# Kernel tuning notes

Hardware: AMD Instinct MI355X
Metric: run time of the kernel (lower is better)

The kernel has to match this reference:

```python
import jax, jax.numpy as jnp
import numpy as np

VOCAB, D_IN, D_H, D_OUT = 32000, 512, 1024, 32000
B, S = 64, 512

def setup_inputs() -> dict:
    key = jax.random.key(0)
    ks = jax.random.split(key, 6)
    xav = lambda k, shp: jax.random.uniform(k, shp, jnp.float32, -1.0, 1.0) * np.sqrt(6.0 / (shp[0] + shp[1]))
    return {
        "tokens": jax.random.randint(ks[0], (B, S), 0, VOCAB),
        "h0": jnp.zeros((B, D_H), jnp.float32),
        "embed_table": jax.random.normal(ks[1], (VOCAB, D_IN), jnp.float32),
        "W_ih": xav(ks[2], (D_IN, D_H)),
        "W_hh": xav(ks[3], (D_H, D_H)),
        "bias_hh": jnp.zeros((D_H,), jnp.float32),
        "W_out": xav(ks[4], (D_H, D_OUT)),
        "b_out": jnp.zeros((D_OUT,), jnp.float32),
    }

def reference(tokens, h0, embed_table, W_ih, W_hh, bias_hh, W_out, b_out):
    # embed: [B,S,D_in] -> seq-first [S,B,D_in]
    x = embed_table[tokens].transpose(1, 0, 2)
    # precompute input projection for all timesteps (one big GEMM)
    xw = jnp.einsum("sbi,ih->sbh", x, W_ih) + bias_hh

    def step(h, xw_t):
        h_new = jnp.tanh(xw_t + h @ W_hh)
        return h_new, None

    h_last, _ = jax.lax.scan(step, h0, xw)
    y_pred = h_last @ W_out + b_out  # [B, D_OUT]
    return y_pred
```

## Files before the change

kernel.cpp:

```cpp
#include <hip/hip_runtime.h>

#define D_IN 512
#define D_H 1024
#define D_OUT 32000
#define NB 64
#define NS 512

typedef __attribute__((ext_vector_type(8))) short short8;
typedef __attribute__((ext_vector_type(8))) __bf16 bf16x8;
typedef __attribute__((ext_vector_type(4))) float f32x4;

__device__ __forceinline__ unsigned short f2bf(float f) {
  unsigned int u = __float_as_uint(f);
  u += 0x7fffu + ((u >> 16) & 1u);
  return (unsigned short)(u >> 16);
}
__device__ __forceinline__ float bf2f(unsigned short s) {
  return __uint_as_float(((unsigned int)s) << 16);
}

__device__ __forceinline__ f32x4 mfma_bf16(short8 a, short8 b, f32x4 c) {
  return __builtin_amdgcn_mfma_f32_16x16x32_bf16(
      __builtin_bit_cast(bf16x8, a), __builtin_bit_cast(bf16x8, b), c, 0, 0, 0);
}

union HQ { unsigned long long q[2]; short8 s; };

__global__ __launch_bounds__(256) void rnn_init(const float* __restrict__ h0,
                                                unsigned short* __restrict__ hex,
                                                unsigned int* __restrict__ flags) {
  int idx = blockIdx.x * 256 + threadIdx.x;
  int bg = idx >> 10;
  int k = idx & 1023;
  int g = bg >> 4, bl = bg & 15;
  float v = h0[idx];
  unsigned short hh = f2bf(v);
  unsigned short hl = f2bf(v - bf2f(hh));
  size_t base = ((size_t)(g * 2 + 0) * 2) * 16384 + (size_t)bl * 1024 + k;
  hex[base] = hh;
  hex[base + 16384] = hl;
  if (blockIdx.x == 0) flags[threadIdx.x] = 0u;
}

__global__ __launch_bounds__(256) void rnn_pack_wih(const float* __restrict__ W_ih,
                                                    unsigned short* __restrict__ bhi,
                                                    unsigned short* __restrict__ blo) {
  int idx = blockIdx.x * 256 + threadIdx.x;
  int j = idx & 7;
  int l = (idx >> 3) & 63;
  int kc = (idx >> 9) & 15;
  int nc = idx >> 13;
  int k = kc * 32 + ((l >> 4) << 3) + j;
  int n = nc * 16 + (l & 15);
  float v = W_ih[(size_t)k * D_H + n];
  unsigned short h = f2bf(v);
  bhi[idx] = h;
  blo[idx] = f2bf(v - bf2f(h));
}

__global__ __launch_bounds__(256) void rnn_stage1(const int* __restrict__ tokens,
                                                  const float* __restrict__ embed,
                                                  const unsigned short* __restrict__ bhi,
                                                  const unsigned short* __restrict__ blo,
                                                  const float* __restrict__ bias,
                                                  float* __restrict__ xw) {
  int bx = blockIdx.x;
  int mt = bx >> 4, nt = bx & 15;
  int tid = threadIdx.x;
  int w = tid >> 6, l = tid & 63;
  int q = l >> 4;

  int m = mt * 64 + w * 16 + (l & 15);
  int b = m & 63, t = m >> 6;
  int tok = tokens[b * NS + t];
  const float* arow = embed + (size_t)tok * D_IN;

  f32x4 acc[4];
#pragma unroll
  for (int i = 0; i < 4; ++i) acc[i] = (f32x4){0.f, 0.f, 0.f, 0.f};

  for (int c = 0; c < 16; ++c) {
    const float* ap = arow + c * 32 + q * 8;
    float4 f0 = *(const float4*)ap;
    float4 f1 = *(const float4*)(ap + 4);
    float fa[8] = {f0.x, f0.y, f0.z, f0.w, f1.x, f1.y, f1.z, f1.w};
    short8 ahi, alo;
#pragma unroll
    for (int j = 0; j < 8; ++j) {
      unsigned short hh = f2bf(fa[j]);
      ahi[j] = (short)hh;
      alo[j] = (short)f2bf(fa[j] - bf2f(hh));
    }
#pragma unroll
    for (int ni = 0; ni < 4; ++ni) {
      int ncg = nt * 4 + ni;
      size_t boff = ((size_t)(ncg * 16 + c) * 64 + l) * 8;
      short8 bh = *(const short8*)(bhi + boff);
      short8 bl_ = *(const short8*)(blo + boff);
      acc[ni] = mfma_bf16(ahi, bh, acc[ni]);
      acc[ni] = mfma_bf16(alo, bh, acc[ni]);
      acc[ni] = mfma_bf16(ahi, bl_, acc[ni]);
    }
  }

#pragma unroll
  for (int ni = 0; ni < 4; ++ni) {
    int col = nt * 64 + ni * 16 + (l & 15);
    float bv = bias[col];
#pragma unroll
    for (int r = 0; r < 4; ++r) {
      int row = mt * 64 + w * 16 + q * 4 + r;
      xw[(size_t)row * D_H + col] = acc[ni][r] + bv;
    }
  }
}

__global__ __launch_bounds__(256, 1) void rnn_recur(const float* __restrict__ xw,
                                                    const float* __restrict__ W_hh,
                                                    unsigned short* __restrict__ hex,
                                                    unsigned int* __restrict__ flags,
                                                    float* __restrict__ h_last) {
  __shared__ short Whi[32768];
  __shared__ short Wlo[32768];
  __shared__ float red[4][16][33];

  const int tid = threadIdx.x;
  const int bx = blockIdx.x;
  const int g = bx >> 5;
  const int jt = bx & 31;
  const int jcol0 = jt * 32;
  const int w = tid >> 6;
  const int l = tid & 63;
  const int q = l >> 4;
  const int b_lane = l & 15;

  for (int v = tid; v < 32768; v += 256) {
    int j = v & 7;
    int ll = (v >> 3) & 63;
    int c = (v >> 9) & 31;
    int s = v >> 14;
    int k = c * 32 + ((ll >> 4) << 3) + j;
    int n = s * 16 + (ll & 15);
    float wv = W_hh[(size_t)k * D_H + jcol0 + n];
    unsigned short hh = f2bf(wv);
    Whi[v] = (short)hh;
    Wlo[v] = (short)f2bf(wv - bf2f(hh));
  }
  __syncthreads();

  unsigned int* flg = flags + g * 32;

  const int be = tid >> 4;
  const int je2 = (tid & 15) * 2;
  const int brow = g * 16 + be;

  for (int t = 1; t <= NS; ++t) {
    const float* xwp = xw + ((size_t)(t - 1) * 64 + brow) * D_H + jcol0 + je2;
    float xv0 = xwp[0];
    float xv1 = xwp[1];

    if (tid < 64) {
      unsigned int target = (unsigned int)(t - 1);
      while (1) {
        unsigned int v = __hip_atomic_load(&flg[l & 31], __ATOMIC_RELAXED,
                                           __HIP_MEMORY_SCOPE_AGENT);
        if (__all((int)(v >= target))) break;
      }
    }
    __syncthreads();

    int rbuf = (t - 1) & 1;
    const unsigned long long* hhi =
        (const unsigned long long*)(hex + ((size_t)(g * 2 + rbuf) * 2 + 0) * 16384);
    const unsigned long long* hlo =
        (const unsigned long long*)(hex + ((size_t)(g * 2 + rbuf) * 2 + 1) * 16384);

    HQ ha[8], hl_[8];
#pragma unroll
    for (int i = 0; i < 8; ++i) {
      int c = w * 8 + i;
      int k = c * 32 + q * 8;
      size_t qi = ((size_t)b_lane * 1024 + k) >> 2;
      ha[i].q[0] = __hip_atomic_load(hhi + qi, __ATOMIC_RELAXED, __HIP_MEMORY_SCOPE_AGENT);
      ha[i].q[1] = __hip_atomic_load(hhi + qi + 1, __ATOMIC_RELAXED, __HIP_MEMORY_SCOPE_AGENT);
      hl_[i].q[0] = __hip_atomic_load(hlo + qi, __ATOMIC_RELAXED, __HIP_MEMORY_SCOPE_AGENT);
      hl_[i].q[1] = __hip_atomic_load(hlo + qi + 1, __ATOMIC_RELAXED, __HIP_MEMORY_SCOPE_AGENT);
    }

    f32x4 a00 = {0.f, 0.f, 0.f, 0.f}, a01 = a00, a02 = a00;
    f32x4 a10 = a00, a11 = a00, a12 = a00;
#pragma unroll
    for (int i = 0; i < 8; ++i) {
      int c = w * 8 + i;
      short8 bh0 = *(const short8*)(Whi + c * 512 + l * 8);
      short8 bl0 = *(const short8*)(Wlo + c * 512 + l * 8);
      short8 bh1 = *(const short8*)(Whi + 16384 + c * 512 + l * 8);
      short8 bl1 = *(const short8*)(Wlo + 16384 + c * 512 + l * 8);
      a00 = mfma_bf16(ha[i].s, bh0, a00);
      a01 = mfma_bf16(hl_[i].s, bh0, a01);
      a02 = mfma_bf16(ha[i].s, bl0, a02);
      a10 = mfma_bf16(ha[i].s, bh1, a10);
      a11 = mfma_bf16(hl_[i].s, bh1, a11);
      a12 = mfma_bf16(ha[i].s, bl1, a12);
    }
    f32x4 s0 = a00 + a01 + a02;
    f32x4 s1 = a10 + a11 + a12;
#pragma unroll
    for (int r = 0; r < 4; ++r) {
      red[w][q * 4 + r][b_lane] = s0[r];
      red[w][q * 4 + r][16 + b_lane] = s1[r];
    }
    __syncthreads();

    float z0 = red[0][be][je2] + red[1][be][je2] + red[2][be][je2] +
               red[3][be][je2] + xv0;
    float z1 = red[0][be][je2 + 1] + red[1][be][je2 + 1] + red[2][be][je2 + 1] +
               red[3][be][je2 + 1] + xv1;
    float hv0 = tanhf(z0);
    float hv1 = tanhf(z1);
    unsigned short h0h = f2bf(hv0), h1h = f2bf(hv1);
    unsigned short h0l = f2bf(hv0 - bf2f(h0h)), h1l = f2bf(hv1 - bf2f(h1h));
    int wbuf = t & 1;
    size_t obase = (size_t)be * 1024 + jcol0 + je2;
    unsigned int* dhi =
        (unsigned int*)(hex + ((size_t)(g * 2 + wbuf) * 2 + 0) * 16384 + obase);
    unsigned int* dlo =
        (unsigned int*)(hex + ((size_t)(g * 2 + wbuf) * 2 + 1) * 16384 + obase);
    unsigned int phi = (unsigned int)h0h | ((unsigned int)h1h << 16);
    unsigned int plo = (unsigned int)h0l | ((unsigned int)h1l << 16);
    __hip_atomic_store(dhi, phi, __ATOMIC_RELAXED, __HIP_MEMORY_SCOPE_AGENT);
    __hip_atomic_store(dlo, plo, __ATOMIC_RELAXED, __HIP_MEMORY_SCOPE_AGENT);
    if (t == NS) {
      h_last[(size_t)brow * 1024 + jcol0 + je2] = hv0;
      h_last[(size_t)brow * 1024 + jcol0 + je2 + 1] = hv1;
    }

    asm volatile("s_waitcnt vmcnt(0)" ::: "memory");
    __syncthreads();
    if (tid == 0)
      __hip_atomic_store(&flg[jt], (unsigned int)t, __ATOMIC_RELAXED,
                         __HIP_MEMORY_SCOPE_AGENT);
  }
}

__global__ __launch_bounds__(256, 2) void rnn_out(const float* __restrict__ h_last,
                                                  const float* __restrict__ W_out,
                                                  const float* __restrict__ b_out,
                                                  float* __restrict__ out) {
  __shared__ float smem[16384];
  int tid = threadIdx.x;
  int jl = tid & 127;
  int kh = tid >> 7;
  int j = blockIdx.x * 128 + jl;

  float acc[64];
#pragma unroll
  for (int b = 0; b < 64; ++b) acc[b] = 0.f;

  for (int kc = 0; kc < 4; ++kc) {
    __syncthreads();
    for (int v = tid; v < 16384; v += 256) {
      int kh2 = v >> 13;
      int b = (v >> 7) & 63;
      int kk = v & 127;
      smem[v] = h_last[(size_t)b * 1024 + kh2 * 512 + kc * 128 + kk];
    }
    __syncthreads();
    int kbase = kh * 512 + kc * 128;
    for (int kkc = 0; kkc < 16; ++kkc) {
      float wreg[8];
#pragma unroll
      for (int i = 0; i < 8; ++i)
        wreg[i] = W_out[(size_t)(kbase + kkc * 8 + i) * D_OUT + j];
#pragma unroll
      for (int b = 0; b < 64; ++b) {
        const float* hp = &smem[kh * 8192 + b * 128 + kkc * 8];
#pragma unroll
        for (int i = 0; i < 8; ++i) acc[b] += hp[i] * wreg[i];
      }
    }
  }
  __syncthreads();
  if (kh == 1) {
#pragma unroll
    for (int b = 0; b < 64; ++b) smem[jl * 65 + b] = acc[b];
  }
  __syncthreads();
  if (kh == 0) {
    float bo = b_out[j];
#pragma unroll
    for (int b = 0; b < 64; ++b)
      out[(size_t)b * D_OUT + j] = acc[b] + smem[jl * 65 + b] + bo;
  }
}

extern "C" void kernel_launch(void* const* d_in, const int* in_sizes, int n_in,
                              void* d_out, int out_size, void* d_ws, size_t ws_size,
                              hipStream_t stream) {
  const int* tokens = (const int*)d_in[0];
  const float* h0 = (const float*)d_in[1];
  const float* embed = (const float*)d_in[2];
  const float* W_ih = (const float*)d_in[3];
  const float* W_hh = (const float*)d_in[4];
  const float* bias_hh = (const float*)d_in[5];
  const float* W_out = (const float*)d_in[6];
  const float* b_out = (const float*)d_in[7];
  float* out = (float*)d_out;

  char* ws = (char*)d_ws;
  float* xw = (float*)(ws);
  unsigned short* wih_hi = (unsigned short*)(ws + 134217728);
  unsigned short* wih_lo = (unsigned short*)(ws + 135266304);
  unsigned short* hex = (unsigned short*)(ws + 136314880);
  unsigned int* flags = (unsigned int*)(ws + 136839168);
  float* h_last = (float*)(ws + 136840192);

  rnn_init<<<256, 256, 0, stream>>>(h0, hex, flags);
  rnn_pack_wih<<<2048, 256, 0, stream>>>(W_ih, wih_hi, wih_lo);
  rnn_stage1<<<8192, 256, 0, stream>>>(tokens, embed, wih_hi, wih_lo, bias_hh, xw);
  rnn_recur<<<128, 256, 0, stream>>>(xw, W_hh, hex, flags, h_last);
  rnn_out<<<250, 256, 0, stream>>>(h_last, W_out, b_out, out);
}
```

Measured before the change: 3.592 ms.

## Consume hidden-state chunks as producer flags arrive instead of waiting for all

Each wave now polls only the eight producer flags for the K-chunks it consumes. It loads and runs MFMAs on whichever chunks are ready, rather than the whole block spinning until all 32 producers finish and then syncing. The hidden-state exchange buffer is re-laid out so that each producer's 32-column slice, with its hi and lo parts, is contiguous at 2 KB per chunk. The xw load for the next step is prefetched during the previous step. This overlaps computation with the remaining synchronisation wait, but adds a dynamic, masked loop that may raise register pressure and branching.

```diff
diff --git a/kernel.cpp b/kernel.cpp
--- a/kernel.cpp
+++ b/kernel.cpp
@@ -33,12 +33,13 @@
   int bg = idx >> 10;
   int k = idx & 1023;
   int g = bg >> 4, bl = bg & 15;
+  int c = k >> 5, kk = k & 31;
   float v = h0[idx];
   unsigned short hh = f2bf(v);
   unsigned short hl = f2bf(v - bf2f(hh));
-  size_t base = ((size_t)(g * 2 + 0) * 2) * 16384 + (size_t)bl * 1024 + k;
+  size_t base = (size_t)(g * 2) * 32768 + (size_t)c * 1024 + bl * 32 + kk;
   hex[base] = hh;
-  hex[base + 16384] = hl;
+  hex[base + 512] = hl;
   if (blockIdx.x == 0) flags[threadIdx.x] = 0u;
 }
 
@@ -149,60 +150,71 @@
   __syncthreads();
 
   unsigned int* flg = flags + g * 32;
+  const int fidx = w * 8 + (l & 7);
+  const unsigned own = ((jt >> 3) == w) ? (1u << (jt & 7)) : 0u;
+  const int loff = b_lane * 64 + q * 16;
 
   const int be = tid >> 4;
   const int je2 = (tid & 15) * 2;
   const int brow = g * 16 + be;
 
+  char* hexb = (char*)hex;
+
+  float xv0, xv1;
+  {
+    const float* xwp = xw + ((size_t)0 * 64 + brow) * D_H + jcol0 + je2;
+    xv0 = xwp[0];
+    xv1 = xwp[1];
+  }
+
   for (int t = 1; t <= NS; ++t) {
-    const float* xwp = xw + ((size_t)(t - 1) * 64 + brow) * D_H + jcol0 + je2;
-    float xv0 = xwp[0];
-    float xv1 = xwp[1];
-
-    if (tid < 64) {
-      unsigned int target = (unsigned int)(t - 1);
-      while (1) {
-        unsigned int v = __hip_atomic_load(&flg[l & 31], __ATOMIC_RELAXED,
-                                           __HIP_MEMORY_SCOPE_AGENT);
-        if (__all((int)(v >= target))) break;
-      }
-    }
-    __syncthreads();
-
-    int rbuf = (t - 1) & 1;
-    const unsigned long long* hhi =
-        (const unsigned long long*)(hex + ((size_t)(g * 2 + rbuf) * 2 + 0) * 16384);
-    const unsigned long long* hlo =
-        (const unsigned long long*)(hex + ((size_t)(g * 2 + rbuf) * 2 + 1) * 16384);
-
-    HQ ha[8], hl_[8];
-#pragma unroll
-    for (int i = 0; i < 8; ++i) {
-      int c = w * 8 + i;
-      int k = c * 32 + q * 8;
-      size_t qi = ((size_t)b_lane * 1024 + k) >> 2;
-      ha[i].q[0] = __hip_atomic_load(hhi + qi, __ATOMIC_RELAXED, __HIP_MEMORY_SCOPE_AGENT);
-      ha[i].q[1] = __hip_atomic_load(hhi + qi + 1, __ATOMIC_RELAXED, __HIP_MEMORY_SCOPE_AGENT);
-      hl_[i].q[0] = __hip_atomic_load(hlo + qi, __ATOMIC_RELAXED, __HIP_MEMORY_SCOPE_AGENT);
-      hl_[i].q[1] = __hip_atomic_load(hlo + qi + 1, __ATOMIC_RELAXED, __HIP_MEMORY_SCOPE_AGENT);
-    }
+    const unsigned target = (unsigned)(t - 1);
+    const char* hb = hexb + (size_t)(g * 2 + ((t - 1) & 1)) * 65536;
 
     f32x4 a00 = {0.f, 0.f, 0.f, 0.f}, a01 = a00, a02 = a00;
     f32x4 a10 = a00, a11 = a00, a12 = a00;
-#pragma unroll
-    for (int i = 0; i < 8; ++i) {
-      int c = w * 8 + i;
-      short8 bh0 = *(const short8*)(Whi + c * 512 + l * 8);
-      short8 bl0 = *(const short8*)(Wlo + c * 512 + l * 8);
-      short8 bh1 = *(const short8*)(Whi + 16384 + c * 512 + l * 8);
-      short8 bl1 = *(const short8*)(Wlo + 16384 + c * 512 + l * 8);
-      a00 = mfma_bf16(ha[i].s, bh0, a00);
-      a01 = mfma_bf16(hl_[i].s, bh0, a01);
-      a02 = mfma_bf16(ha[i].s, bl0, a02);
-      a10 = mfma_bf16(ha[i].s, bh1, a10);
-      a11 = mfma_bf16(hl_[i].s, bh1, a11);
-      a12 = mfma_bf16(ha[i].s, bl1, a12);
-    }
+
+    unsigned done = 0u;
+    while (done != 255u) {
+      unsigned int fv = __hip_atomic_load(&flg[fidx], __ATOMIC_RELAXED,
+                                          __HIP_MEMORY_SCOPE_AGENT);
+      unsigned rdy = (((unsigned)__ballot((int)(fv >= target))) & 255u) | own;
+      unsigned avail = rdy & ~done;
+      if (avail == 0u) continue;
+      done |= avail;
+
+      HQ ha_[8], hl_[8];
+#pragma unroll
+      for (int i = 0; i < 8; ++i) {
+        if (avail & (1u << i)) {
+          const char* cb = hb + (size_t)(w * 8 + i) * 2048;
+          const unsigned long long* ph = (const unsigned long long*)(cb + loff);
+          const unsigned long long* pl = (const unsigned long long*)(cb + 1024 + loff);
+          ha_[i].q[0] = __hip_atomic_load(ph, __ATOMIC_RELAXED, __HIP_MEMORY_SCOPE_AGENT);
+          ha_[i].q[1] = __hip_atomic_load(ph + 1, __ATOMIC_RELAXED, __HIP_MEMORY_SCOPE_AGENT);
+          hl_[i].q[0] = __hip_atomic_load(pl, __ATOMIC_RELAXED, __HIP_MEMORY_SCOPE_AGENT);
+          hl_[i].q[1] = __hip_atomic_load(pl + 1, __ATOMIC_RELAXED, __HIP_MEMORY_SCOPE_AGENT);
+        }
+      }
+      __builtin_amdgcn_sched_barrier(0);
+#pragma unroll
+      for (int i = 0; i < 8; ++i) {
+        if (avail & (1u << i)) {
+          int c = w * 8 + i;
+          short8 bh0 = *(const short8*)(Whi + c * 512 + l * 8);
+          short8 bl0 = *(const short8*)(Wlo + c * 512 + l * 8);
+          short8 bh1 = *(const short8*)(Whi + 16384 + c * 512 + l * 8);
+          short8 bl1 = *(const short8*)(Wlo + 16384 + c * 512 + l * 8);
+          a00 = mfma_bf16(ha_[i].s, bh0, a00);
+          a01 = mfma_bf16(hl_[i].s, bh0, a01);
+          a02 = mfma_bf16(ha_[i].s, bl0, a02);
+          a10 = mfma_bf16(ha_[i].s, bh1, a10);
+          a11 = mfma_bf16(hl_[i].s, bh1, a11);
+          a12 = mfma_bf16(ha_[i].s, bl1, a12);
+        }
+      }
+    }
+
     f32x4 s0 = a00 + a01 + a02;
     f32x4 s1 = a10 + a11 + a12;
 #pragma unroll
@@ -220,12 +232,9 @@
     float hv1 = tanhf(z1);
     unsigned short h0h = f2bf(hv0), h1h = f2bf(hv1);
     unsigned short h0l = f2bf(hv0 - bf2f(h0h)), h1l = f2bf(hv1 - bf2f(h1h));
-    int wbuf = t & 1;
-    size_t obase = (size_t)be * 1024 + jcol0 + je2;
-    unsigned int* dhi =
-        (unsigned int*)(hex + ((size_t)(g * 2 + wbuf) * 2 + 0) * 16384 + obase);
-    unsigned int* dlo =
-        (unsigned int*)(hex + ((size_t)(g * 2 + wbuf) * 2 + 1) * 16384 + obase);
+    char* wb = hexb + (size_t)(g * 2 + (t & 1)) * 65536 + (size_t)jt * 2048;
+    unsigned int* dhi = (unsigned int*)(wb + be * 64 + je2 * 2);
+    unsigned int* dlo = (unsigned int*)(wb + 1024 + be * 64 + je2 * 2);
     unsigned int phi = (unsigned int)h0h | ((unsigned int)h1h << 16);
     unsigned int plo = (unsigned int)h0l | ((unsigned int)h1l << 16);
     __hip_atomic_store(dhi, phi, __ATOMIC_RELAXED, __HIP_MEMORY_SCOPE_AGENT);
@@ -236,6 +245,11 @@
     }
 
     asm volatile("s_waitcnt vmcnt(0)" ::: "memory");
+    if (t < NS) {
+      const float* xwp = xw + ((size_t)t * 64 + brow) * D_H + jcol0 + je2;
+      xv0 = xwp[0];
+      xv1 = xwp[1];
+    }
     __syncthreads();
     if (tid == 0)
       __hip_atomic_store(&flg[jt], (unsigned int)t, __ATOMIC_RELAXED,
```

New measurement: 2.968 ms. -17.4%, faster.
